# Kernel optimization log

Measured on AMD Instinct MI355X. Metric: run time of the kernel, lower is better.

The kernel has to match this reference:

```python
import jax, jax.numpy as jnp
import numpy as np

B, E, H, V, D2, T = 128, 512, 512, 32000, 1024, 17

def setup_inputs() -> dict:
    key = jax.random.key(0)
    ks = jax.random.split(key, 13)
    s = 0.02
    return {
        "features": jax.random.normal(ks[0], (B, 512), dtype=jnp.float32),
        "captions": jax.random.randint(ks[1], (B, T), 0, V, dtype=jnp.int32),
        "W_enc": jax.random.normal(ks[2], (512, E), dtype=jnp.float32) * s,
        "b_enc": jnp.zeros((E,), dtype=jnp.float32),
        "emb": jax.random.normal(ks[3], (V, E), dtype=jnp.float32) * s,
        "W_ih": jax.random.normal(ks[4], (4 * H, E), dtype=jnp.float32) * s,
        "b_ih": jnp.zeros((4 * H,), dtype=jnp.float32),
        "W_hh": jax.random.normal(ks[5], (4 * H, H), dtype=jnp.float32) * s,
        "b_hh": jnp.zeros((4 * H,), dtype=jnp.float32),
        "W_d2": jax.random.normal(ks[6], (H, D2), dtype=jnp.float32) * s,
        "b_d2": jnp.zeros((D2,), dtype=jnp.float32),
        "W_last": jax.random.normal(ks[7], (D2, V), dtype=jnp.float32) * s,
        "b_last": jnp.zeros((V,), dtype=jnp.float32),
    }


def reference(features, captions, W_enc, b_enc, emb, W_ih, b_ih, W_hh, b_hh, W_d2, b_d2, W_last, b_last):
    # encoder_last: project frozen-resnet features [B,512] -> [B,E]
    feat = features @ W_enc + b_enc
    # embed captions[:, :-1] -> [B,16,E], prepend image feature -> [B,17,E]
    e = emb[captions[:, :-1]]
    x = jnp.concatenate([feat[:, None, :], e], axis=1)  # [B,T,E]

    def step(carry, xt):
        h, c = carry
        gates = xt @ W_ih.T + b_ih + h @ W_hh.T + b_hh  # [B,4H]
        i, f, g, o = jnp.split(gates, 4, axis=-1)  # PyTorch LSTMCell gate order
        i, f, o = jax.nn.sigmoid(i), jax.nn.sigmoid(f), jax.nn.sigmoid(o)
        g = jnp.tanh(g)
        c = f * c + i * g
        h = o * jnp.tanh(c)
        return (h, c), h

    h0 = jnp.zeros((x.shape[0], H), dtype=x.dtype)
    c0 = jnp.zeros((x.shape[0], H), dtype=x.dtype)
    _, hs = jax.lax.scan(step, (h0, c0), jnp.swapaxes(x, 0, 1))  # [T,B,H]
    hs = jnp.swapaxes(hs, 0, 1)  # [B,T,H]

    out = jax.nn.relu(hs @ W_d2 + b_d2)       # [B,T,D2]
    logits = out @ W_last + b_last            # [B,T,V]
    return jax.nn.softmax(logits, axis=2)
```

## Files before the change

kernel.cpp:

```cpp
#include <hip/hip_runtime.h>
#include <hip/hip_bf16.h>

#define B_   128
#define T_   17
#define E_   512
#define H_   512
#define V_   32000
#define D2_  1024
#define MR_  (B_*T_)

typedef __attribute__((ext_vector_type(8))) short short8;
typedef __attribute__((ext_vector_type(4))) float f32x4;

__device__ __forceinline__ unsigned short f2b(float f) {
  unsigned u = __float_as_uint(f);
  u += 0x7FFFu + ((u >> 16) & 1u);
  return (unsigned short)(u >> 16);
}
__device__ __forceinline__ float sigf(float x) { return 1.f / (1.f + __expf(-x)); }
__device__ __forceinline__ float tanhfast(float x) {
  x = fminf(fmaxf(x, -15.f), 15.f);
  float e = __expf(2.f * x);
  return (e - 1.f) / (e + 1.f);
}

__device__ __forceinline__ void async16(const void* g, void* l) {
  __builtin_amdgcn_global_load_lds((const __attribute__((address_space(1))) unsigned int*)g,
                                   (__attribute__((address_space(3))) unsigned int*)l,
                                   16, 0, 0);
}

template<int EPI, int SWZ>
__global__ __launch_bounds__(256, 2)
void gemm_bt(const unsigned short* __restrict__ A,
             const unsigned short* __restrict__ Bt,
             void* __restrict__ C,
             const float* __restrict__ bias0,
             const float* __restrict__ bias1,
             int N, int K, int nbm, int nwork)
{
  __shared__ unsigned short sA[128 * 32];
  __shared__ unsigned short sB[128 * 32];

  int f = blockIdx.x;
  if constexpr (SWZ) {
    int per = (nwork + 7) >> 3;
    f = (f & 7) * per + (f >> 3);
    if (f >= nwork) return;
  }
  const size_t bm = (size_t)(f % nbm) * 128;
  const size_t bn = (size_t)(f / nbm) * 128;

  const int tid  = threadIdx.x;
  const int lane = tid & 63;
  const int wave = tid >> 6;
  const int wm   = wave & 1;
  const int wn   = wave >> 1;

  const int sRow   = wave * 32 + (lane >> 2);
  const int gchunk = (lane & 3) ^ ((sRow >> 2) & 3);

  const unsigned short* gA  = A  + (bm + sRow)      * (size_t)K + gchunk * 8;
  const unsigned short* gA2 = A  + (bm + sRow + 16) * (size_t)K + gchunk * 8;
  const unsigned short* gB  = Bt + (bn + sRow)      * (size_t)K + gchunk * 8;
  const unsigned short* gB2 = Bt + (bn + sRow + 16) * (size_t)K + gchunk * 8;

  unsigned short* lA  = &sA[wave * 1024];
  unsigned short* lA2 = &sA[wave * 1024 + 512];
  unsigned short* lB  = &sB[wave * 1024];
  unsigned short* lB2 = &sB[wave * 1024 + 512];

  f32x4 acc[4][4] = {};
  const int fm = lane & 15;
  const int q  = lane >> 4;

  for (int kt = 0; kt < K; kt += 32) {
    async16(gA  + kt, lA);
    async16(gA2 + kt, lA2);
    async16(gB  + kt, lB);
    async16(gB2 + kt, lB2);
    __syncthreads();

    short8 af[4], bfv[4];
#pragma unroll
    for (int i = 0; i < 4; i++) {
      int ra = wm * 64 + i * 16 + fm;
      af[i]  = *(const short8*)&sA[ra * 32 + ((q ^ ((ra >> 2) & 3)) * 8)];
      int rb = wn * 64 + i * 16 + fm;
      bfv[i] = *(const short8*)&sB[rb * 32 + ((q ^ ((rb >> 2) & 3)) * 8)];
    }
#pragma unroll
    for (int i = 0; i < 4; i++)
#pragma unroll
      for (int j = 0; j < 4; j++)
        acc[i][j] = __builtin_amdgcn_mfma_f32_16x16x32_bf16(af[i], bfv[j], acc[i][j], 0, 0, 0);
    __syncthreads();
  }

#pragma unroll
  for (int i = 0; i < 4; i++) {
#pragma unroll
    for (int j = 0; j < 4; j++) {
      size_t col = bn + wn * 64 + j * 16 + fm;
      float bv = 0.f;
      if constexpr (EPI == 0) {
        size_t oc = ((col & 3) << 9) + (col >> 2);
        bv = bias0[oc] + bias1[oc];
      }
      if constexpr (EPI == 2 || EPI == 3 || EPI == 4) bv = bias0[col];
#pragma unroll
      for (int r = 0; r < 4; r++) {
        size_t row = bm + wm * 64 + i * 16 + q * 4 + r;
        float v = acc[i][j][r] + bv;
        if constexpr (EPI == 2) {
          v = v > 0.f ? v : 0.f;
          ((unsigned short*)C)[row * N + col] = f2b(v);
        } else if constexpr (EPI == 3) {
          ((unsigned short*)C)[row * N + col] = f2b(v);
        } else {
          ((float*)C)[row * N + col] = v;
        }
      }
    }
  }
}

#define STG(gp, lb, row0, kt) do { \
    async16((gp) + (size_t)(row0) * K + (kt),       (lb) + (row0) * 64); \
    async16((gp) + (size_t)((row0) + 8) * K + (kt), (lb) + ((row0) + 8) * 64); \
  } while (0)

#define LDA(dst, sa_, mq_) do { \
    _Pragma("unroll") \
    for (int ff = 0; ff < 2; ff++) { \
      const int r_ = wm * 128 + ((mq_) * 2 + ff) * 16 + fm; \
      _Pragma("unroll") \
      for (int ks = 0; ks < 2; ks++) \
        dst[ff][ks] = *(const short8*)&(sa_)[r_ * 64 + (((ks * 4 + q) ^ (r_ & 7)) << 3)]; \
    } } while (0)

#define LDB(dst, sb_) do { \
    _Pragma("unroll") \
    for (int j = 0; j < 4; j++) { \
      const int r_ = wn * 64 + j * 16 + fm; \
      _Pragma("unroll") \
      for (int ks = 0; ks < 2; ks++) \
        dst[j][ks] = *(const short8*)&(sb_)[r_ * 64 + (((ks * 4 + q) ^ (r_ & 7)) << 3)]; \
    } } while (0)

#define MMA(ab, mq_) do { \
    _Pragma("unroll") \
    for (int ff = 0; ff < 2; ff++) \
      _Pragma("unroll") \
      for (int j = 0; j < 4; j++) \
        _Pragma("unroll") \
        for (int ks = 0; ks < 2; ks++) \
          acc[(mq_) * 2 + ff][j] = __builtin_amdgcn_mfma_f32_16x16x32_bf16( \
              ab[ff][ks], breg[j][ks], acc[(mq_) * 2 + ff][j], 0, 0, 0); \
  } while (0)

#define PH_TAIL() do { \
    asm volatile("s_waitcnt lgkmcnt(0)" ::: "memory"); \
    __builtin_amdgcn_sched_barrier(0); \
    __builtin_amdgcn_s_barrier(); \
  } while (0)

#define TILE(BI, T) do { \
    const int t_ = (T); \
    const int kt1 = (t_ + 1) << 6, kt2 = (t_ + 2) << 6; \
    const bool st1 = (t_ + 1) < NT, st2 = (t_ + 2) < NT; \
     \
    LDA(af1, sA[BI], 1); \
    if (st1) STG(gA, sA[(BI) ^ 1], arow1, kt1); \
    __builtin_amdgcn_sched_barrier(0); \
    __builtin_amdgcn_s_setprio(1); MMA(af0, 0); __builtin_amdgcn_s_setprio(0); \
    PH_TAIL(); \
     \
    LDA(af0, sA[BI], 2); \
    if (st2) STG(gB, sB[BI], brow0, kt2); \
    __builtin_amdgcn_sched_barrier(0); \
    __builtin_amdgcn_s_setprio(1); MMA(af1, 1); __builtin_amdgcn_s_setprio(0); \
    PH_TAIL(); \
     \
    LDA(af1, sA[BI], 3); \
    if (st2) STG(gB, sB[BI], brow1, kt2); \
    __builtin_amdgcn_sched_barrier(0); \
    __builtin_amdgcn_s_setprio(1); MMA(af0, 2); __builtin_amdgcn_s_setprio(0); \
    asm volatile("s_waitcnt lgkmcnt(0)" ::: "memory"); \
    if (st2) { asm volatile("s_waitcnt vmcnt(4)" ::: "memory"); } \
    else     { asm volatile("s_waitcnt vmcnt(0)" ::: "memory"); } \
    __builtin_amdgcn_sched_barrier(0); \
    __builtin_amdgcn_s_barrier(); \
     \
    if (st1) LDA(af0, sA[(BI) ^ 1], 0); \
    if (st2) STG(gA, sA[BI], arow0, kt2); \
    __builtin_amdgcn_sched_barrier(0); \
    __builtin_amdgcn_s_setprio(1); MMA(af1, 3); __builtin_amdgcn_s_setprio(0); \
    if (st1) LDB(breg, sB[(BI) ^ 1]); \
    PH_TAIL(); \
  } while (0)

template<int EPI>
__global__ __launch_bounds__(512, 2)
void gemm256(const unsigned short* __restrict__ A,
             const unsigned short* __restrict__ Bt,
             void* __restrict__ C,
             const float* __restrict__ bias0,
             int N, int K, int M, int nbm, int nwork)
{
  __shared__ unsigned short sA[2][256 * 64];
  __shared__ unsigned short sB[2][256 * 64];

  int f = blockIdx.x;
  const int per = (nwork + 7) >> 3;
  f = (f & 7) * per + (f >> 3);
  if (f >= nwork) return;
  int bmx = (f % nbm) * 256;
  if (bmx > M - 256) bmx = M - 256;
  const size_t bm = (size_t)bmx;
  const size_t bn = (size_t)(f / nbm) * 256;

  const int tid  = threadIdx.x;
  const int lane = tid & 63;
  const int wave = tid >> 6;
  const int wm   = wave >> 2;
  const int wn   = wave & 3;
  const int fm   = lane & 15;
  const int q    = lane >> 4;

  const int cs = (((lane & 7) ^ (lane >> 3)) << 3);
  const unsigned short* gA = A  + (bm + (lane >> 3)) * (size_t)K + cs;
  const unsigned short* gB = Bt + (bn + (lane >> 3)) * (size_t)K + cs;

  const int NT = K >> 6;
  const int arow0 = (wave & 3) * 16 + (wave >> 2) * 128;
  const int arow1 = arow0 + 64;
  const int brow0 = wave * 16;
  const int brow1 = brow0 + 128;

  STG(gB, sB[0], brow0, 0);
  STG(gB, sB[0], brow1, 0);
  STG(gA, sA[0], arow0, 0);
  STG(gA, sA[0], arow1, 0);
  if (NT > 1) {
    STG(gB, sB[1], brow0, 64);
    STG(gB, sB[1], brow1, 64);
    STG(gA, sA[1], arow0, 64);
    asm volatile("s_waitcnt vmcnt(6)" ::: "memory");
  } else {
    asm volatile("s_waitcnt vmcnt(0)" ::: "memory");
  }
  __builtin_amdgcn_s_barrier();

  f32x4 acc[8][4] = {};
  short8 af0[2][2], af1[2][2];
  short8 breg[4][2];

  LDA(af0, sA[0], 0);
  LDB(breg, sB[0]);
  asm volatile("s_waitcnt lgkmcnt(0)" ::: "memory");
  __builtin_amdgcn_sched_barrier(0);

  for (int tt = 0; tt < NT; tt += 2) {
    TILE(0, tt);
    TILE(1, tt + 1);
  }

#pragma unroll
  for (int i = 0; i < 8; i++) {
#pragma unroll
    for (int j = 0; j < 4; j++) {
      const size_t col = bn + wn * 64 + j * 16 + fm;
      const float bv = bias0[col];
#pragma unroll
      for (int r = 0; r < 4; r++) {
        const size_t row = bm + wm * 128 + i * 16 + q * 4 + r;
        const float v = acc[i][j][r] + bv;
        if constexpr (EPI == 3) ((unsigned short*)C)[row * (size_t)N + col] = f2b(v);
        else                    ((float*)C)[row * (size_t)N + col] = v;
      }
    }
  }
}
#undef TILE
#undef PH_TAIL
#undef MMA
#undef LDB
#undef LDA
#undef STG

__global__ __launch_bounds__(256)
void lstm_step(const unsigned short* __restrict__ hprev,
               const unsigned short* __restrict__ Whh,
               const float* __restrict__ Gt,
               float* __restrict__ c,
               unsigned short* __restrict__ hout,
               unsigned short* __restrict__ hsb,
               int t)
{
  __shared__ char smem[131072];
  unsigned short* sA = (unsigned short*)smem;
  unsigned short* sB = (unsigned short*)(smem + 65536);
  float* gl = (float*)smem;

  const int tid  = threadIdx.x;
  const int lane = tid & 63;
  const int wave = tid >> 6;
  const int wm   = wave & 1;
  const int wn   = wave >> 1;
  const int n0   = blockIdx.x * 128;

  const int lr = lane >> 5;
  const int lp = lane & 31;

  f32x4 acc[4][4] = {};
  const int fm = lane & 15;
  const int q  = lane >> 4;

  for (int kt = 0; kt < 512; kt += 256) {
#pragma unroll
    for (int s = 0; s < 16; s++) {
      int row = wave * 32 + s * 2 + lr;
      int gch = lp ^ (row & 7);
      async16(hprev + (size_t)row * 512 + kt + gch * 8,
              sA + wave * 8192 + s * 512 + lane * 8);
      async16(Whh + (size_t)(n0 + row) * 512 + kt + gch * 8,
              sB + wave * 8192 + s * 512 + lane * 8);
    }
    __syncthreads();

#pragma unroll
    for (int kk = 0; kk < 8; kk++) {
      int ch = kk * 4 + q;
      short8 af[4], bfv[4];
#pragma unroll
      for (int i = 0; i < 4; i++) {
        int ra = wm * 64 + i * 16 + fm;
        af[i]  = *(const short8*)&sA[ra * 256 + ((ch ^ (ra & 7)) * 8)];
        int rb = wn * 64 + i * 16 + fm;
        bfv[i] = *(const short8*)&sB[rb * 256 + ((ch ^ (rb & 7)) * 8)];
      }
#pragma unroll
      for (int i = 0; i < 4; i++)
#pragma unroll
        for (int j = 0; j < 4; j++)
          acc[i][j] = __builtin_amdgcn_mfma_f32_16x16x32_bf16(af[i], bfv[j], acc[i][j], 0, 0, 0);
    }
    __syncthreads();
  }

#pragma unroll
  for (int i = 0; i < 4; i++)
#pragma unroll
    for (int j = 0; j < 4; j++)
#pragma unroll
      for (int r = 0; r < 4; r++)
        gl[(wm * 64 + i * 16 + q * 4 + r) * 132 + wn * 64 + j * 16 + fm] = acc[i][j][r];
  __syncthreads();

#pragma unroll
  for (int it = 0; it < 16; it++) {
    int p   = it * 256 + tid;
    int row = p >> 5;
    int ul  = p & 31;
    float4 a4 = *(float4*)&gl[row * 132 + ul * 4];
    float4 G4 = *(const float4*)&Gt[row * 2048 + n0 + ul * 4];
    float gi = a4.x + G4.x, gf = a4.y + G4.y, gg = a4.z + G4.z, go = a4.w + G4.w;
    int gu  = (n0 >> 2) + ul;
    int idx = row * 512 + gu;
    float cn = sigf(gf) * c[idx] + sigf(gi) * tanhfast(gg);
    c[idx] = cn;
    float hn = sigf(go) * tanhfast(cn);
    unsigned short h16 = f2b(hn);
    hout[idx] = h16;
    hsb[((size_t)row * T_ + t) * 512 + gu] = h16;
  }
}

__global__ void lstm_point0(const float* __restrict__ G0, float* __restrict__ c,
                            unsigned short* __restrict__ hb, unsigned short* __restrict__ hsb) {
  int idx = blockIdx.x * 256 + threadIdx.x;
  int b = idx >> 9, u = idx & 511;
  float4 g4 = ((const float4*)(G0 + (size_t)b * 2048))[u];
  float cn = sigf(g4.x) * tanhfast(g4.z);
  c[idx] = cn;
  float hn = sigf(g4.w) * tanhfast(cn);
  unsigned short h16 = f2b(hn);
  hb[idx] = h16;
  hsb[((size_t)b * T_ + 0) * 512 + u] = h16;
}

__global__ void permute_cvt2(const float* __restrict__ Wih, const float* __restrict__ Whh,
                             unsigned short* __restrict__ dih, unsigned short* __restrict__ dhh) {
  int p = blockIdx.x;
  const float* src = (p < 2048) ? Wih : Whh;
  unsigned short* dst = (p < 2048) ? dih : dhh;
  int pp = p & 2047;
  int ir = ((pp & 3) << 9) + (pp >> 2);
  float4 v = ((const float4*)(src + (size_t)ir * 512))[threadIdx.x];
  ushort4 o;
  o.x = f2b(v.x); o.y = f2b(v.y); o.z = f2b(v.z); o.w = f2b(v.w);
  ((ushort4*)(dst + (size_t)p * 512))[threadIdx.x] = o;
}

__global__ void transpose_cvt(const float* __restrict__ src, unsigned short* __restrict__ dst,
                              int K, int N) {
  __shared__ float tile[32][33];
  int n0 = blockIdx.x * 32, k0 = blockIdx.y * 32;
  int tcol = threadIdx.x & 31, trow = threadIdx.x >> 5;
  for (int r = trow; r < 32; r += 8)
    tile[r][tcol] = src[(size_t)(k0 + r) * N + n0 + tcol];
  __syncthreads();
  for (int r = trow; r < 32; r += 8)
    dst[(size_t)(n0 + r) * K + k0 + tcol] = f2b(tile[tcol][r]);
}

__global__ __launch_bounds__(256) void encode(const float* __restrict__ features,
                                              const float* __restrict__ W_enc,
                                              const float* __restrict__ b_enc,
                                              unsigned short* __restrict__ xb) {
  __shared__ float fs[512];
  int b = blockIdx.y, e = blockIdx.x * 256 + threadIdx.x;
  fs[threadIdx.x]       = features[b * 512 + threadIdx.x];
  fs[threadIdx.x + 256] = features[b * 512 + threadIdx.x + 256];
  __syncthreads();
  float acc = 0.f;
#pragma unroll 8
  for (int k = 0; k < 512; k++) acc += fs[k] * W_enc[(size_t)k * 512 + e];
  xb[(size_t)b * 512 + e] = f2b(acc + b_enc[e]);
}

__global__ void embed_k(const int* __restrict__ captions, const float* __restrict__ emb,
                        unsigned short* __restrict__ xb) {
  int t = blockIdx.x + 1, b = blockIdx.y;
  int tok = captions[b * T_ + (t - 1)];
  float4 v = ((const float4*)(emb + (size_t)tok * 512))[threadIdx.x];
  ushort4 o;
  o.x = f2b(v.x); o.y = f2b(v.y); o.z = f2b(v.z); o.w = f2b(v.w);
  ((ushort4*)(xb + (size_t)(t * B_ + b) * 512))[threadIdx.x] = o;
}

__global__ __launch_bounds__(1024) void softmax_b(const unsigned short* __restrict__ lg,
                                                  float* __restrict__ out) {
  __shared__ float ps[1024];
  const uint4* r4 = (const uint4*)(lg + (size_t)blockIdx.x * V_);
  float* orow = out + (size_t)blockIdx.x * V_;
  int tid = threadIdx.x;
  float v[4][8];
  float s = 0.f;
#pragma unroll
  for (int u = 0; u < 4; u++) {
    int i = u * 1024 + tid;
    if (i < 4000) {
      uint4 w = r4[i];
      unsigned a[4] = {w.x, w.y, w.z, w.w};
#pragma unroll
      for (int k = 0; k < 4; k++) {
        float lo = __uint_as_float(a[k] << 16);
        float hi = __uint_as_float(a[k] & 0xffff0000u);
        float e0 = __expf(lo), e1 = __expf(hi);
        v[u][2 * k] = e0; v[u][2 * k + 1] = e1;
        s += e0 + e1;
      }
    }
  }
  ps[tid] = s;
  __syncthreads();
  for (int o = 512; o > 0; o >>= 1) {
    if (tid < o) ps[tid] += ps[tid + o];
    __syncthreads();
  }
  float inv = 1.f / ps[0];
#pragma unroll
  for (int u = 0; u < 4; u++) {
    int i = u * 1024 + tid;
    if (i < 4000) {
      float4 o1 = {v[u][0] * inv, v[u][1] * inv, v[u][2] * inv, v[u][3] * inv};
      float4 o2 = {v[u][4] * inv, v[u][5] * inv, v[u][6] * inv, v[u][7] * inv};
      ((float4*)(orow + (size_t)i * 8))[0] = o1;
      ((float4*)(orow + (size_t)i * 8))[1] = o2;
    }
  }
}

__global__ __launch_bounds__(1024) void softmax_f(float* __restrict__ out) {
  __shared__ float ps[1024];
  float* r = out + (size_t)blockIdx.x * V_;
  int tid = threadIdx.x;
  float v[32];
  float s = 0.f;
#pragma unroll
  for (int u = 0; u < 32; u++) {
    int i = u * 1024 + tid;
    if (i < V_) { float e = __expf(r[i]); v[u] = e; s += e; }
  }
  ps[tid] = s;
  __syncthreads();
  for (int o = 512; o > 0; o >>= 1) {
    if (tid < o) ps[tid] += ps[tid + o];
    __syncthreads();
  }
  float inv = 1.f / ps[0];
#pragma unroll
  for (int u = 0; u < 32; u++) {
    int i = u * 1024 + tid;
    if (i < V_) r[i] = v[u] * inv;
  }
}

extern "C" void kernel_launch(void* const* d_in, const int* in_sizes, int n_in,
                              void* d_out, int out_size, void* d_ws, size_t ws_size,
                              hipStream_t stream) {
  const float* features = (const float*)d_in[0];
  const int*   captions = (const int*)d_in[1];
  const float* W_enc  = (const float*)d_in[2];
  const float* b_enc  = (const float*)d_in[3];
  const float* emb    = (const float*)d_in[4];
  const float* W_ih   = (const float*)d_in[5];
  const float* b_ih   = (const float*)d_in[6];
  const float* W_hh   = (const float*)d_in[7];
  const float* b_hh   = (const float*)d_in[8];
  const float* W_d2   = (const float*)d_in[9];
  const float* b_d2   = (const float*)d_in[10];
  const float* W_last = (const float*)d_in[11];
  const float* b_last = (const float*)d_in[12];
  float* out = (float*)d_out;

  char* ws = (char*)d_ws;
  size_t off = 0;
  auto alloc = [&](size_t bytes) -> void* {
    void* p = ws + off;
    off += (bytes + 255) & ~(size_t)255;
    return p;
  };
  unsigned short* xb     = (unsigned short*)alloc((size_t)MR_ * E_ * 2);
  unsigned short* Wb_ih  = (unsigned short*)alloc((size_t)4 * H_ * E_ * 2);
  unsigned short* Wb_hh  = (unsigned short*)alloc((size_t)4 * H_ * H_ * 2);
  unsigned short* Wb_d2t = (unsigned short*)alloc((size_t)D2_ * H_ * 2);
  unsigned short* Wb_lt  = (unsigned short*)alloc((size_t)V_ * D2_ * 2);
  float*          G      = (float*)alloc((size_t)MR_ * 4 * H_ * 4);
  float*          cst    = (float*)alloc((size_t)B_ * H_ * 4);
  unsigned short* hb0    = (unsigned short*)alloc((size_t)B_ * H_ * 2);
  unsigned short* hb1    = (unsigned short*)alloc((size_t)B_ * H_ * 2);
  unsigned short* hsb    = (unsigned short*)alloc((size_t)MR_ * H_ * 2);
  unsigned short* outb   = (unsigned short*)alloc((size_t)MR_ * D2_ * 2);
  unsigned short* lgb    = (unsigned short*)alloc((size_t)MR_ * V_ * 2);
  const bool bf16_logits = (off <= ws_size);
  (void)in_sizes; (void)n_in; (void)out_size;

  permute_cvt2<<<4096, 128, 0, stream>>>(W_ih, W_hh, Wb_ih, Wb_hh);
  transpose_cvt<<<dim3(D2_ / 32, H_ / 32), 256, 0, stream>>>(W_d2, Wb_d2t, H_, D2_);

  encode<<<dim3(2, B_), 256, 0, stream>>>(features, W_enc, b_enc, xb);
  embed_k<<<dim3(T_ - 1, B_), 128, 0, stream>>>(captions, emb, xb);

  gemm_bt<0, 0><<<17 * 16, 256, 0, stream>>>(xb, Wb_ih, G, b_ih, b_hh, 4 * H_, E_, 17, 17 * 16);

  lstm_point0<<<B_ * H_ / 256, 256, 0, stream>>>(G, cst, hb0, hsb);
  for (int t = 1; t < T_; t++) {
    unsigned short* hp = (t & 1) ? hb0 : hb1;
    unsigned short* hc = (t & 1) ? hb1 : hb0;
    lstm_step<<<16, 256, 0, stream>>>(hp, Wb_hh, G + (size_t)t * B_ * 4 * H_, cst, hc, hsb, t);
  }

  transpose_cvt<<<dim3(V_ / 32, D2_ / 32), 256, 0, stream>>>(W_last, Wb_lt, D2_, V_);

  gemm_bt<2, 0><<<17 * 8, 256, 0, stream>>>(hsb, Wb_d2t, outb, b_d2, nullptr, D2_, H_, 17, 17 * 8);

  const int nbm2   = 9;
  const int nwork2 = nbm2 * (V_ / 256);
  const int per2   = (nwork2 + 7) / 8;
  if (bf16_logits) {
    gemm256<3><<<8 * per2, 512, 0, stream>>>(outb, Wb_lt, lgb, b_last, V_, D2_, MR_, nbm2, nwork2);
    softmax_b<<<MR_, 1024, 0, stream>>>(lgb, out);
  } else {
    gemm256<4><<<8 * per2, 512, 0, stream>>>(outb, Wb_lt, out, b_last, V_, D2_, MR_, nbm2, nwork2);
    softmax_f<<<MR_, 1024, 0, stream>>>(out);
  }
}
```

Measured before the change: 937.3 us.

## Shrink logits GEMM M-tile to 128 rows and interleave B-fragment loads with MFMAs

Changes the vocab-projection GEMM tile from 256x256 to 128x256 so that M=2176 divides exactly into 17 tiles, eliminating the clamped overlapping last row tile that recomputed rows. The software pipeline is reworked for the smaller A tile: fewer A fragments per wave, rescheduled async global-to-LDS staging and wait counts, and next-tile B fragment loads interleaved with the final MFMA group. Smaller accumulator and LDS footprint may help occupancy, at the cost of lower arithmetic intensity per B tile load.

Result: slower. 981.4 us (+4.7%).

```diff
diff --git a/kernel.cpp b/kernel.cpp
--- a/kernel.cpp
+++ b/kernel.cpp
@@ -125,19 +125,19 @@
   }
 }
 
-#define STG(gp, lb, row0, kt) do { \
+#define STG2(gp, lb, row0, kt) do { \
     async16((gp) + (size_t)(row0) * K + (kt),       (lb) + (row0) * 64); \
     async16((gp) + (size_t)((row0) + 8) * K + (kt), (lb) + ((row0) + 8) * 64); \
   } while (0)
 
-#define LDA(dst, sa_, mq_) do { \
-    _Pragma("unroll") \
-    for (int ff = 0; ff < 2; ff++) { \
-      const int r_ = wm * 128 + ((mq_) * 2 + ff) * 16 + fm; \
-      _Pragma("unroll") \
-      for (int ks = 0; ks < 2; ks++) \
-        dst[ff][ks] = *(const short8*)&(sa_)[r_ * 64 + (((ks * 4 + q) ^ (r_ & 7)) << 3)]; \
-    } } while (0)
+#define STG1(gp, lb, row0, kt) \
+    async16((gp) + (size_t)(row0) * K + (kt), (lb) + (row0) * 64)
+
+#define LDA1(dst, sa_, mf_) do { \
+    const int r_ = wm * 64 + (mf_) * 16 + fm; \
+    dst[0] = *(const short8*)&(sa_)[r_ * 64 + (((q) ^ (r_ & 7)) << 3)]; \
+    dst[1] = *(const short8*)&(sa_)[r_ * 64 + (((4 + q) ^ (r_ & 7)) << 3)]; \
+  } while (0)
 
 #define LDB(dst, sb_) do { \
     _Pragma("unroll") \
@@ -148,15 +148,13 @@
         dst[j][ks] = *(const short8*)&(sb_)[r_ * 64 + (((ks * 4 + q) ^ (r_ & 7)) << 3)]; \
     } } while (0)
 
-#define MMA(ab, mq_) do { \
+#define MMA(ab, mf_) do { \
     _Pragma("unroll") \
-    for (int ff = 0; ff < 2; ff++) \
+    for (int j = 0; j < 4; j++) \
       _Pragma("unroll") \
-      for (int j = 0; j < 4; j++) \
-        _Pragma("unroll") \
-        for (int ks = 0; ks < 2; ks++) \
-          acc[(mq_) * 2 + ff][j] = __builtin_amdgcn_mfma_f32_16x16x32_bf16( \
-              ab[ff][ks], breg[j][ks], acc[(mq_) * 2 + ff][j], 0, 0, 0); \
+      for (int ks = 0; ks < 2; ks++) \
+        acc[mf_][j] = __builtin_amdgcn_mfma_f32_16x16x32_bf16( \
+            ab[ks], breg[j][ks], acc[mf_][j], 0, 0, 0); \
   } while (0)
 
 #define PH_TAIL() do { \
@@ -167,36 +165,46 @@
 
 #define TILE(BI, T) do { \
     const int t_ = (T); \
-    const int kt1 = (t_ + 1) << 6, kt2 = (t_ + 2) << 6; \
+    const int kt2 = (t_ + 2) << 6; \
     const bool st1 = (t_ + 1) < NT, st2 = (t_ + 2) < NT; \
      \
-    LDA(af1, sA[BI], 1); \
-    if (st1) STG(gA, sA[(BI) ^ 1], arow1, kt1); \
+    LDA1(af1, sA[BI], 1); \
+    if (st2) STG2(gB, sB[BI], brow, kt2); \
     __builtin_amdgcn_sched_barrier(0); \
     __builtin_amdgcn_s_setprio(1); MMA(af0, 0); __builtin_amdgcn_s_setprio(0); \
     PH_TAIL(); \
      \
-    LDA(af0, sA[BI], 2); \
-    if (st2) STG(gB, sB[BI], brow0, kt2); \
+    LDA1(af0, sA[BI], 2); \
+    if (st2) STG2(gB, sB[BI], brow + 128, kt2); \
     __builtin_amdgcn_sched_barrier(0); \
     __builtin_amdgcn_s_setprio(1); MMA(af1, 1); __builtin_amdgcn_s_setprio(0); \
     PH_TAIL(); \
      \
-    LDA(af1, sA[BI], 3); \
-    if (st2) STG(gB, sB[BI], brow1, kt2); \
+    LDA1(af1, sA[BI], 3); \
+    if (st2) STG1(gA, sA[BI], arow, kt2); \
     __builtin_amdgcn_sched_barrier(0); \
     __builtin_amdgcn_s_setprio(1); MMA(af0, 2); __builtin_amdgcn_s_setprio(0); \
     asm volatile("s_waitcnt lgkmcnt(0)" ::: "memory"); \
-    if (st2) { asm volatile("s_waitcnt vmcnt(4)" ::: "memory"); } \
+    if (st2) { asm volatile("s_waitcnt vmcnt(5)" ::: "memory"); } \
     else     { asm volatile("s_waitcnt vmcnt(0)" ::: "memory"); } \
     __builtin_amdgcn_sched_barrier(0); \
     __builtin_amdgcn_s_barrier(); \
      \
-    if (st1) LDA(af0, sA[(BI) ^ 1], 0); \
-    if (st2) STG(gA, sA[BI], arow0, kt2); \
-    __builtin_amdgcn_sched_barrier(0); \
-    __builtin_amdgcn_s_setprio(1); MMA(af1, 3); __builtin_amdgcn_s_setprio(0); \
-    if (st1) LDB(breg, sB[(BI) ^ 1]); \
+    if (st2) STG1(gA, sA[BI], arow + 64, kt2); \
+    __builtin_amdgcn_s_setprio(1); \
+    { const unsigned short* sBn = sB[(BI) ^ 1]; \
+      _Pragma("unroll") \
+      for (int j = 0; j < 4; j++) { \
+        acc[3][j] = __builtin_amdgcn_mfma_f32_16x16x32_bf16(af1[0], breg[j][0], acc[3][j], 0, 0, 0); \
+        acc[3][j] = __builtin_amdgcn_mfma_f32_16x16x32_bf16(af1[1], breg[j][1], acc[3][j], 0, 0, 0); \
+        if (st1) { \
+          const int r_ = wn * 64 + j * 16 + fm; \
+          breg[j][0] = *(const short8*)&sBn[r_ * 64 + (((q) ^ (r_ & 7)) << 3)]; \
+          breg[j][1] = *(const short8*)&sBn[r_ * 64 + (((4 + q) ^ (r_ & 7)) << 3)]; \
+        } \
+      } } \
+    __builtin_amdgcn_s_setprio(0); \
+    if (st1) LDA1(af0, sA[(BI) ^ 1], 0); \
     PH_TAIL(); \
   } while (0)
 
@@ -206,18 +214,16 @@
              const unsigned short* __restrict__ Bt,
              void* __restrict__ C,
              const float* __restrict__ bias0,
-             int N, int K, int M, int nbm, int nwork)
+             int N, int K, int nbm, int nwork)
 {
-  __shared__ unsigned short sA[2][256 * 64];
+  __shared__ unsigned short sA[2][128 * 64];
   __shared__ unsigned short sB[2][256 * 64];
 
   int f = blockIdx.x;
   const int per = (nwork + 7) >> 3;
   f = (f & 7) * per + (f >> 3);
   if (f >= nwork) return;
-  int bmx = (f % nbm) * 256;
-  if (bmx > M - 256) bmx = M - 256;
-  const size_t bm = (size_t)bmx;
+  const size_t bm = (size_t)(f % nbm) * 128;
   const size_t bn = (size_t)(f / nbm) * 256;
 
   const int tid  = threadIdx.x;
@@ -233,30 +239,29 @@
   const unsigned short* gB = Bt + (bn + (lane >> 3)) * (size_t)K + cs;
 
   const int NT = K >> 6;
-  const int arow0 = (wave & 3) * 16 + (wave >> 2) * 128;
-  const int arow1 = arow0 + 64;
-  const int brow0 = wave * 16;
-  const int brow1 = brow0 + 128;
-
-  STG(gB, sB[0], brow0, 0);
-  STG(gB, sB[0], brow1, 0);
-  STG(gA, sA[0], arow0, 0);
-  STG(gA, sA[0], arow1, 0);
+  const int arow = wave * 8;
+  const int brow = wave * 16;
+
+  STG2(gB, sB[0], brow, 0);
+  STG2(gB, sB[0], brow + 128, 0);
+  STG1(gA, sA[0], arow, 0);
+  STG1(gA, sA[0], arow + 64, 0);
   if (NT > 1) {
-    STG(gB, sB[1], brow0, 64);
-    STG(gB, sB[1], brow1, 64);
-    STG(gA, sA[1], arow0, 64);
+    STG2(gB, sB[1], brow, 64);
+    STG2(gB, sB[1], brow + 128, 64);
+    STG1(gA, sA[1], arow, 64);
+    STG1(gA, sA[1], arow + 64, 64);
     asm volatile("s_waitcnt vmcnt(6)" ::: "memory");
   } else {
     asm volatile("s_waitcnt vmcnt(0)" ::: "memory");
   }
   __builtin_amdgcn_s_barrier();
 
-  f32x4 acc[8][4] = {};
-  short8 af0[2][2], af1[2][2];
+  f32x4 acc[4][4] = {};
+  short8 af0[2], af1[2];
   short8 breg[4][2];
 
-  LDA(af0, sA[0], 0);
+  LDA1(af0, sA[0], 0);
   LDB(breg, sB[0]);
   asm volatile("s_waitcnt lgkmcnt(0)" ::: "memory");
   __builtin_amdgcn_sched_barrier(0);
@@ -267,14 +272,14 @@
   }
 
 #pragma unroll
-  for (int i = 0; i < 8; i++) {
+  for (int i = 0; i < 4; i++) {
 #pragma unroll
     for (int j = 0; j < 4; j++) {
       const size_t col = bn + wn * 64 + j * 16 + fm;
       const float bv = bias0[col];
 #pragma unroll
       for (int r = 0; r < 4; r++) {
-        const size_t row = bm + wm * 128 + i * 16 + q * 4 + r;
+        const size_t row = bm + wm * 64 + i * 16 + q * 4 + r;
         const float v = acc[i][j][r] + bv;
         if constexpr (EPI == 3) ((unsigned short*)C)[row * (size_t)N + col] = f2b(v);
         else                    ((float*)C)[row * (size_t)N + col] = v;
@@ -286,8 +291,9 @@
 #undef PH_TAIL
 #undef MMA
 #undef LDB
-#undef LDA
-#undef STG
+#undef LDA1
+#undef STG1
+#undef STG2
 
 __global__ __launch_bounds__(256)
 void lstm_step(const unsigned short* __restrict__ hprev,
@@ -567,14 +573,14 @@
 
   gemm_bt<2, 0><<<17 * 8, 256, 0, stream>>>(hsb, Wb_d2t, outb, b_d2, nullptr, D2_, H_, 17, 17 * 8);
 
-  const int nbm2   = 9;
+  const int nbm2   = 17;
   const int nwork2 = nbm2 * (V_ / 256);
   const int per2   = (nwork2 + 7) / 8;
   if (bf16_logits) {
-    gemm256<3><<<8 * per2, 512, 0, stream>>>(outb, Wb_lt, lgb, b_last, V_, D2_, MR_, nbm2, nwork2);
+    gemm256<3><<<8 * per2, 512, 0, stream>>>(outb, Wb_lt, lgb, b_last, V_, D2_, nbm2, nwork2);
     softmax_b<<<MR_, 1024, 0, stream>>>(lgb, out);
   } else {
-    gemm256<4><<<8 * per2, 512, 0, stream>>>(outb, Wb_lt, out, b_last, V_, D2_, MR_, nbm2, nwork2);
+    gemm256<4><<<8 * per2, 512, 0, stream>>>(outb, Wb_lt, out, b_last, V_, D2_, nbm2, nwork2);
     softmax_f<<<MR_, 1024, 0, stream>>>(out);
   }
 }
```
